# Kernel optimization log

Measured on AMD Instinct MI355X. Metric: run time of the kernel, lower is better.

## Reference

```python
import jax, jax.numpy as jnp
import numpy as np

N, F_IN, F_OUT, MAX_ORDER = 8192, 128, 128, 2
EDGE_DENSITY = 0.004  # avg degree ~33


def setup_inputs() -> dict:
    key = jax.random.key(0)
    k1, k2, k3, k4 = jax.random.split(key, 4)
    x = jax.random.normal(k1, (N, F_IN), dtype=jnp.float32)
    # dense stack of adjacency powers; layer only cares about the nonzero pattern
    adj_powers = (jax.random.uniform(k2, (MAX_ORDER, N, N)) < EDGE_DENSITY).astype(jnp.float32)
    edge_index = jax.random.randint(k3, (2, 32768), 0, N, dtype=jnp.int64)  # unused by the math
    W = jax.random.normal(k4, (F_IN, F_OUT), dtype=jnp.float32) / np.sqrt(F_IN).astype(np.float32)
    b = jnp.zeros((F_OUT,), dtype=jnp.float32)
    alpha = jnp.ones((MAX_ORDER,), dtype=jnp.float32)
    return {"x": x, "edge_index": edge_index, "adj_powers": adj_powers,
            "W": W, "b": b, "alpha": alpha}


def reference(x, edge_index, adj_powers, W, b, alpha):
    # GCNConv with shared (W, b) applied to each adjacency power's edge set.
    # dense->sparse->dense roundtrip in the original just binarizes the adjacency
    # (every nonzero entry becomes a unit-weight edge).
    xw = x @ W  # [N, F_out], shared across orders
    n = x.shape[0]
    diag = jnp.arange(n)

    def one_order(adj_n):
        A = (adj_n != 0).astype(x.dtype)
        # add_remaining_self_loops with unit weight == force diagonal to 1
        A = A.at[diag, diag].set(1.0)
        deg = A.sum(axis=1)  # [N]
        dinv = jnp.where(deg > 0, jax.lax.rsqrt(deg), 0.0)
        Ahat = dinv[:, None] * A * dinv[None, :]  # D^{-1/2} (A+I) D^{-1/2}
        return Ahat @ xw + b  # [N, F_out]

    per_order = jax.vmap(one_order)(adj_powers)  # [max_order, N, F_out]
    return jnp.einsum("o,onf->nf", alpha, per_order)
```

## Files before the change

kernel.cpp:

```cpp
#include <hip/hip_runtime.h>
#include <math.h>

#define NN 8192
#define FF 128
#define ORD 2
#define CSR_STRIDE 128
#define XW_ROWS 16
#define XW_BLOCKS (NN / XW_ROWS)
#define SCAN_BLOCKS (ORD * NN)

__global__ __launch_bounds__(256) void scan_xw_kernel(
    const float* __restrict__ adj, const float* __restrict__ x,
    const float* __restrict__ W,
    float* __restrict__ xw, float* __restrict__ dinv,
    int* __restrict__ cnt, int* __restrict__ colidx, int csr_ok)
{
    const int t = threadIdx.x;

    if (blockIdx.x < XW_BLOCKS) {
        const int row0 = blockIdx.x * XW_ROWS;
        __shared__ float xsT[FF * 20];
        for (int idx = t; idx < XW_ROWS * FF; idx += 256) {
            const int r = idx >> 7, k = idx & 127;
            xsT[k * 20 + r] = x[(size_t)(row0 + r) * FF + k];
        }
        __syncthreads();
        const int f = t & 127;
        const int h = t >> 7;
        float acc[8];
#pragma unroll
        for (int r = 0; r < 8; ++r) acc[r] = 0.f;
#pragma unroll 4
        for (int k = 0; k < FF; ++k) {
            const float wk = W[k * FF + f];
            const float4* xp = (const float4*)&xsT[k * 20 + h * 8];
            const float4 a0 = xp[0], a1 = xp[1];
            acc[0] += a0.x * wk; acc[1] += a0.y * wk;
            acc[2] += a0.z * wk; acc[3] += a0.w * wk;
            acc[4] += a1.x * wk; acc[5] += a1.y * wk;
            acc[6] += a1.z * wk; acc[7] += a1.w * wk;
        }
#pragma unroll
        for (int r = 0; r < 8; ++r)
            xw[(size_t)(row0 + h * 8 + r) * FF + f] = acc[r];
        return;
    }

    const int bid = blockIdx.x - XW_BLOCKS;
    const int i   = bid & (NN - 1);

    const float4* row = (const float4*)(adj + (size_t)bid * NN);

    unsigned int m = 0;
#pragma unroll
    for (int s = 0; s < 8; ++s) {
        const float4 v = row[s * 256 + t];
        if (v.x != 0.f) m |= 1u << (4 * s + 0);
        if (v.y != 0.f) m |= 1u << (4 * s + 1);
        if (v.z != 0.f) m |= 1u << (4 * s + 2);
        if (v.w != 0.f) m |= 1u << (4 * s + 3);
    }
    if (t == ((i >> 2) & 255)) m &= ~(1u << (((i >> 2) >> 8) * 4 + (i & 3)));

    const int c = __popc(m);

    const int lane = t & 63;
    int incl = c;
#pragma unroll
    for (int d = 1; d < 64; d <<= 1) {
        const int n = __shfl_up(incl, d);
        if (lane >= d) incl += n;
    }
    __shared__ int wtot[4];
    if (lane == 63) wtot[t >> 6] = incl;
    __syncthreads();
    const int w = t >> 6;
    int woff = 0;
#pragma unroll
    for (int ww = 0; ww < 3; ++ww)
        if (ww < w) woff += wtot[ww];
    const int total = wtot[0] + wtot[1] + wtot[2] + wtot[3];
    const int myoff = woff + incl - c;

    if (t == 0) {
        cnt[bid]  = total;
        dinv[bid] = 1.0f / sqrtf((float)(total + 1));
    }

    if (csr_ok && total <= CSR_STRIDE) {
        int* outp = colidx + (size_t)bid * CSR_STRIDE + myoff;
        unsigned int mm = m;
        const int base = 4 * t;
        while (mm) {
            const int b = __builtin_ctz(mm);
            mm &= mm - 1;
            *outp++ = ((b >> 2) << 10) + base + (b & 3);
        }
    }
}

__global__ __launch_bounds__(512) void gather_kernel(
    const float* __restrict__ adj, const float* __restrict__ xw,
    const float* __restrict__ dinv, const int* __restrict__ cnt,
    const int* __restrict__ colidx, const float* __restrict__ bias,
    const float* __restrict__ alpha, float* __restrict__ out, int csr_ok)
{
    const int i = blockIdx.x;
    const int t = threadIdx.x;
    const int l = t & 31;
    const int g = t >> 5;

    __shared__ int    qj[2 * CSR_STRIDE];
    __shared__ float  qw[2 * CSR_STRIDE];
    __shared__ float4 part[16][32];

    const int   c0 = cnt[i],        c1 = cnt[NN + i];
    const float di0 = dinv[i],      di1 = dinv[NN + i];
    const float a0 = alpha[0],      a1 = alpha[1];
    const int   ctot = c0 + c1;
    const int   fits = csr_ok && (c0 <= CSR_STRIDE) && (c1 <= CSR_STRIDE);

    float4 acc = make_float4(0.f, 0.f, 0.f, 0.f);

    if (fits) {
        if (t < ctot) {
            const int o = (t < c0) ? 0 : 1;
            const int e = (o == 0) ? t : t - c0;
            const int j = colidx[(size_t)(o * NN + i) * CSR_STRIDE + e];
            qj[t] = j;
            qw[t] = ((o == 0) ? a0 * di0 : a1 * di1) * dinv[o * NN + j];
        }
        __syncthreads();
        for (int e = g; e < ctot; e += 16) {
            const int   j = qj[e];
            const float w = qw[e];
            const float4 v = *(const float4*)&xw[(size_t)j * FF + 4 * l];
            acc.x += w * v.x; acc.y += w * v.y;
            acc.z += w * v.z; acc.w += w * v.w;
        }
    } else {
        for (int o = 0; o < ORD; ++o) {
            const float  wo   = (o == 0) ? a0 * di0 : a1 * di1;
            const float* rowp = adj + (size_t)(o * NN + i) * NN;
            for (int j = g * (NN / 16); j < (g + 1) * (NN / 16); ++j) {
                const float a = rowp[j];
                if (a != 0.f && j != i) {
                    const float w = wo * dinv[o * NN + j];
                    const float4 v = *(const float4*)&xw[(size_t)j * FF + 4 * l];
                    acc.x += w * v.x; acc.y += w * v.y;
                    acc.z += w * v.z; acc.w += w * v.w;
                }
            }
        }
    }

    part[g][l] = acc;
    __syncthreads();

    if (t < 32) {
        float4 r = part[0][t];
#pragma unroll
        for (int gg = 1; gg < 16; ++gg) {
            const float4 p = part[gg][t];
            r.x += p.x; r.y += p.y; r.z += p.z; r.w += p.w;
        }
        const float coefd = a0 * di0 * di0 + a1 * di1 * di1;
        const float cb    = a0 + a1;
        const float4 xi = *(const float4*)&xw[(size_t)i * FF + 4 * t];
        const float4 bb = *(const float4*)&bias[4 * t];
        r.x += coefd * xi.x + cb * bb.x;
        r.y += coefd * xi.y + cb * bb.y;
        r.z += coefd * xi.z + cb * bb.z;
        r.w += coefd * xi.w + cb * bb.w;
        *(float4*)&out[(size_t)i * FF + 4 * t] = r;
    }
}

extern "C" void kernel_launch(void* const* d_in, const int* in_sizes, int n_in,
                              void* d_out, int out_size, void* d_ws, size_t ws_size,
                              hipStream_t stream) {
    const float* x     = (const float*)d_in[0];
    const float* adj   = (const float*)d_in[2];
    const float* W     = (const float*)d_in[3];
    const float* bias  = (const float*)d_in[4];
    const float* alpha = (const float*)d_in[5];
    float* out         = (float*)d_out;

    char* ws = (char*)d_ws;
    size_t off = 0;
    float* xw     = (float*)(ws + off); off += (size_t)NN * FF * sizeof(float);
    float* dinv   = (float*)(ws + off); off += (size_t)ORD * NN * sizeof(float);
    int*   cnt    = (int*)(ws + off);   off += (size_t)ORD * NN * sizeof(int);
    int*   colidx = (int*)(ws + off);   off += (size_t)ORD * NN * CSR_STRIDE * sizeof(int);
    const int csr_ok = (ws_size >= off) ? 1 : 0;

    hipLaunchKernelGGL(scan_xw_kernel, dim3(XW_BLOCKS + SCAN_BLOCKS), dim3(256), 0, stream,
                       adj, x, W, xw, dinv, cnt, colidx, csr_ok);
    hipLaunchKernelGGL(gather_kernel, dim3(NN), dim3(512), 0, stream,
                       adj, xw, dinv, cnt, colidx, bias, alpha, out, csr_ok);
}
```

Measured before the change: 129.4 us.

## Scan adjacency per wave with persistent rows and gather bf16 xw copy

The adjacency scan moves from one 256-thread block per row to one 64-lane wave per row. It runs on 1024 persistent blocks that each loop over four rows and use only wave-level shuffles, so block barriers go away and each lane keeps more loads in flight. The xw kernel now also writes a bf16 copy of xw, and the gather kernel reads neighbour rows from that copy with 256 threads each handling 8 features. This halves gather traffic but adds rounding error. The final cross-group reduction becomes a tree through shared memory, which adds several barriers.

Result: faster. 125.5 us (-3.0%).

```diff
diff --git a/kernel.cpp b/kernel.cpp
--- a/kernel.cpp
+++ b/kernel.cpp
@@ -7,13 +7,23 @@
 #define CSR_STRIDE 128
 #define XW_ROWS 16
 #define XW_BLOCKS (NN / XW_ROWS)
-#define SCAN_BLOCKS (ORD * NN)
-
-__global__ __launch_bounds__(256) void scan_xw_kernel(
+#define SCAN_BLOCKS 1024
+#define ROWS_PER_WAVE 4
+#define NWAVES (SCAN_BLOCKS * 4)
+
+__device__ __forceinline__ unsigned short f2bf(float v) {
+    const unsigned int u = __float_as_uint(v);
+    return (unsigned short)((u + 0x7FFFu + ((u >> 16) & 1u)) >> 16);
+}
+__device__ __forceinline__ float bflo(unsigned int u) { return __uint_as_float(u << 16); }
+__device__ __forceinline__ float bfhi(unsigned int u) { return __uint_as_float(u & 0xFFFF0000u); }
+
+__global__ __launch_bounds__(256) void kernelA(
     const float* __restrict__ adj, const float* __restrict__ x,
     const float* __restrict__ W,
-    float* __restrict__ xw, float* __restrict__ dinv,
-    int* __restrict__ cnt, int* __restrict__ colidx, int csr_ok)
+    float* __restrict__ xw, unsigned short* __restrict__ xwh,
+    float* __restrict__ dinv, int* __restrict__ cnt,
+    int* __restrict__ colidx, int csr_ok)
 {
     const int t = threadIdx.x;
 
@@ -41,86 +51,106 @@
             acc[6] += a1.z * wk; acc[7] += a1.w * wk;
         }
 #pragma unroll
-        for (int r = 0; r < 8; ++r)
-            xw[(size_t)(row0 + h * 8 + r) * FF + f] = acc[r];
+        for (int r = 0; r < 8; ++r) {
+            const size_t idx = (size_t)(row0 + h * 8 + r) * FF + f;
+            xw[idx]  = acc[r];
+            xwh[idx] = f2bf(acc[r]);
+        }
         return;
     }
 
-    const int bid = blockIdx.x - XW_BLOCKS;
-    const int i   = bid & (NN - 1);
-
-    const float4* row = (const float4*)(adj + (size_t)bid * NN);
-
-    unsigned int m = 0;
-#pragma unroll
-    for (int s = 0; s < 8; ++s) {
-        const float4 v = row[s * 256 + t];
-        if (v.x != 0.f) m |= 1u << (4 * s + 0);
-        if (v.y != 0.f) m |= 1u << (4 * s + 1);
-        if (v.z != 0.f) m |= 1u << (4 * s + 2);
-        if (v.w != 0.f) m |= 1u << (4 * s + 3);
-    }
-    if (t == ((i >> 2) & 255)) m &= ~(1u << (((i >> 2) >> 8) * 4 + (i & 3)));
-
-    const int c = __popc(m);
-
+    const int wave_id = (blockIdx.x - XW_BLOCKS) * 4 + (t >> 6);
     const int lane = t & 63;
-    int incl = c;
-#pragma unroll
-    for (int d = 1; d < 64; d <<= 1) {
-        const int n = __shfl_up(incl, d);
-        if (lane >= d) incl += n;
-    }
-    __shared__ int wtot[4];
-    if (lane == 63) wtot[t >> 6] = incl;
-    __syncthreads();
-    const int w = t >> 6;
-    int woff = 0;
-#pragma unroll
-    for (int ww = 0; ww < 3; ++ww)
-        if (ww < w) woff += wtot[ww];
-    const int total = wtot[0] + wtot[1] + wtot[2] + wtot[3];
-    const int myoff = woff + incl - c;
-
-    if (t == 0) {
-        cnt[bid]  = total;
-        dinv[bid] = 1.0f / sqrtf((float)(total + 1));
-    }
-
-    if (csr_ok && total <= CSR_STRIDE) {
-        int* outp = colidx + (size_t)bid * CSR_STRIDE + myoff;
-        unsigned int mm = m;
-        const int base = 4 * t;
-        while (mm) {
-            const int b = __builtin_ctz(mm);
-            mm &= mm - 1;
-            *outp++ = ((b >> 2) << 10) + base + (b & 3);
-        }
-    }
-}
-
-__global__ __launch_bounds__(512) void gather_kernel(
+    const int b4l  = 4 * lane;
+
+#pragma unroll 1
+    for (int k = 0; k < ROWS_PER_WAVE; ++k) {
+        const int r = k * NWAVES + wave_id;
+        const int i = r & (NN - 1);
+        const float4* rowp = (const float4*)(adj + (size_t)r * NN);
+
+        unsigned int m[4];
+#pragma unroll
+        for (int ch = 0; ch < 4; ++ch) {
+            float4 v[8];
+#pragma unroll
+            for (int s = 0; s < 8; ++s) v[s] = rowp[ch * 512 + s * 64 + lane];
+            unsigned int mm = 0;
+#pragma unroll
+            for (int s = 0; s < 8; ++s) {
+                if (v[s].x != 0.f) mm |= 1u << (4 * s + 0);
+                if (v[s].y != 0.f) mm |= 1u << (4 * s + 1);
+                if (v[s].z != 0.f) mm |= 1u << (4 * s + 2);
+                if (v[s].w != 0.f) mm |= 1u << (4 * s + 3);
+            }
+            m[ch] = mm;
+        }
+
+        {
+            const int p_i    = i >> 2;
+            const int lane_i = p_i & 63;
+            const int ch_i   = p_i >> 9;
+            const unsigned int bit = 1u << (4 * ((p_i >> 6) & 7) + (i & 3));
+#pragma unroll
+            for (int ch = 0; ch < 4; ++ch)
+                if (ch == ch_i && lane == lane_i) m[ch] &= ~bit;
+        }
+
+        const int c = __popc(m[0]) + __popc(m[1]) + __popc(m[2]) + __popc(m[3]);
+
+        int incl = c;
+#pragma unroll
+        for (int d = 1; d < 64; d <<= 1) {
+            const int n = __shfl_up(incl, d);
+            if (lane >= d) incl += n;
+        }
+        const int total = __shfl(incl, 63);
+
+        if (lane == 0) {
+            cnt[r]  = total;
+            dinv[r] = 1.0f / sqrtf((float)(total + 1));
+        }
+
+        if (csr_ok && total <= CSR_STRIDE) {
+            int* outp = colidx + (size_t)r * CSR_STRIDE + (incl - c);
+#pragma unroll
+            for (int ch = 0; ch < 4; ++ch) {
+                unsigned int mm = m[ch];
+                while (mm) {
+                    const int bq = __builtin_ctz(mm);
+                    mm &= mm - 1;
+                    *outp++ = ch * 2048 + ((bq >> 2) << 8) + b4l + (bq & 3);
+                }
+            }
+        }
+    }
+}
+
+__global__ __launch_bounds__(256) void kernelB(
     const float* __restrict__ adj, const float* __restrict__ xw,
+    const unsigned short* __restrict__ xwh,
     const float* __restrict__ dinv, const int* __restrict__ cnt,
     const int* __restrict__ colidx, const float* __restrict__ bias,
     const float* __restrict__ alpha, float* __restrict__ out, int csr_ok)
 {
-    const int i = blockIdx.x;
-    const int t = threadIdx.x;
-    const int l = t & 31;
-    const int g = t >> 5;
-
-    __shared__ int    qj[2 * CSR_STRIDE];
-    __shared__ float  qw[2 * CSR_STRIDE];
-    __shared__ float4 part[16][32];
-
-    const int   c0 = cnt[i],        c1 = cnt[NN + i];
-    const float di0 = dinv[i],      di1 = dinv[NN + i];
-    const float a0 = alpha[0],      a1 = alpha[1];
+    const int i  = blockIdx.x;
+    const int t  = threadIdx.x;
+    const int fb = t & 15;
+    const int g  = t >> 4;
+
+    __shared__ int   qj[2 * CSR_STRIDE];
+    __shared__ float qw[2 * CSR_STRIDE];
+    __shared__ float part[16][16][8];
+
+    const int   c0  = cnt[i],  c1  = cnt[NN + i];
+    const float di0 = dinv[i], di1 = dinv[NN + i];
+    const float a0  = alpha[0], a1 = alpha[1];
     const int   ctot = c0 + c1;
     const int   fits = csr_ok && (c0 <= CSR_STRIDE) && (c1 <= CSR_STRIDE);
 
-    float4 acc = make_float4(0.f, 0.f, 0.f, 0.f);
+    float acc[8];
+#pragma unroll
+    for (int c = 0; c < 8; ++c) acc[c] = 0.f;
 
     if (fits) {
         if (t < ctot) {
@@ -134,9 +164,11 @@
         for (int e = g; e < ctot; e += 16) {
             const int   j = qj[e];
             const float w = qw[e];
-            const float4 v = *(const float4*)&xw[(size_t)j * FF + 4 * l];
-            acc.x += w * v.x; acc.y += w * v.y;
-            acc.z += w * v.z; acc.w += w * v.w;
+            const uint4 u = *(const uint4*)&xwh[(size_t)j * FF + 8 * fb];
+            acc[0] += w * bflo(u.x); acc[1] += w * bfhi(u.x);
+            acc[2] += w * bflo(u.y); acc[3] += w * bfhi(u.y);
+            acc[4] += w * bflo(u.z); acc[5] += w * bfhi(u.z);
+            acc[6] += w * bflo(u.w); acc[7] += w * bfhi(u.w);
         }
     } else {
         for (int o = 0; o < ORD; ++o) {
@@ -146,33 +178,38 @@
                 const float a = rowp[j];
                 if (a != 0.f && j != i) {
                     const float w = wo * dinv[o * NN + j];
-                    const float4 v = *(const float4*)&xw[(size_t)j * FF + 4 * l];
-                    acc.x += w * v.x; acc.y += w * v.y;
-                    acc.z += w * v.z; acc.w += w * v.w;
+                    const float* xr = &xw[(size_t)j * FF + 8 * fb];
+#pragma unroll
+                    for (int c = 0; c < 8; ++c) acc[c] += w * xr[c];
                 }
             }
         }
     }
 
-    part[g][l] = acc;
+#pragma unroll
+    for (int c = 0; c < 8; ++c) part[g][fb][c] = acc[c];
     __syncthreads();
 
-    if (t < 32) {
-        float4 r = part[0][t];
-#pragma unroll
-        for (int gg = 1; gg < 16; ++gg) {
-            const float4 p = part[gg][t];
-            r.x += p.x; r.y += p.y; r.z += p.z; r.w += p.w;
-        }
+#pragma unroll
+    for (int step = 8; step >= 1; step >>= 1) {
+        if (g < step) {
+#pragma unroll
+            for (int c = 0; c < 8; ++c) part[g][fb][c] += part[g + step][fb][c];
+        }
+        __syncthreads();
+    }
+
+    if (t < 16) {
         const float coefd = a0 * di0 * di0 + a1 * di1 * di1;
         const float cb    = a0 + a1;
-        const float4 xi = *(const float4*)&xw[(size_t)i * FF + 4 * t];
-        const float4 bb = *(const float4*)&bias[4 * t];
-        r.x += coefd * xi.x + cb * bb.x;
-        r.y += coefd * xi.y + cb * bb.y;
-        r.z += coefd * xi.z + cb * bb.z;
-        r.w += coefd * xi.w + cb * bb.w;
-        *(float4*)&out[(size_t)i * FF + 4 * t] = r;
+        const float* xi = &xw[(size_t)i * FF + 8 * t];
+        const float* bb = &bias[8 * t];
+        float r[8];
+#pragma unroll
+        for (int c = 0; c < 8; ++c)
+            r[c] = part[0][t][c] + coefd * xi[c] + cb * bb[c];
+        *(float4*)&out[(size_t)i * FF + 8 * t]     = make_float4(r[0], r[1], r[2], r[3]);
+        *(float4*)&out[(size_t)i * FF + 8 * t + 4] = make_float4(r[4], r[5], r[6], r[7]);
     }
 }
 
@@ -188,14 +225,15 @@
 
     char* ws = (char*)d_ws;
     size_t off = 0;
-    float* xw     = (float*)(ws + off); off += (size_t)NN * FF * sizeof(float);
-    float* dinv   = (float*)(ws + off); off += (size_t)ORD * NN * sizeof(float);
-    int*   cnt    = (int*)(ws + off);   off += (size_t)ORD * NN * sizeof(int);
-    int*   colidx = (int*)(ws + off);   off += (size_t)ORD * NN * CSR_STRIDE * sizeof(int);
+    float*          xw     = (float*)(ws + off); off += (size_t)NN * FF * sizeof(float);
+    unsigned short* xwh    = (unsigned short*)(ws + off); off += (size_t)NN * FF * sizeof(short);
+    float*          dinv   = (float*)(ws + off); off += (size_t)ORD * NN * sizeof(float);
+    int*            cnt    = (int*)(ws + off);   off += (size_t)ORD * NN * sizeof(int);
+    int*            colidx = (int*)(ws + off);   off += (size_t)ORD * NN * CSR_STRIDE * sizeof(int);
     const int csr_ok = (ws_size >= off) ? 1 : 0;
 
-    hipLaunchKernelGGL(scan_xw_kernel, dim3(XW_BLOCKS + SCAN_BLOCKS), dim3(256), 0, stream,
-                       adj, x, W, xw, dinv, cnt, colidx, csr_ok);
-    hipLaunchKernelGGL(gather_kernel, dim3(NN), dim3(512), 0, stream,
-                       adj, xw, dinv, cnt, colidx, bias, alpha, out, csr_ok);
-}
+    hipLaunchKernelGGL(kernelA, dim3(XW_BLOCKS + SCAN_BLOCKS), dim3(256), 0, stream,
+                       adj, x, W, xw, xwh, dinv, cnt, colidx, csr_ok);
+    hipLaunchKernelGGL(kernelB, dim3(NN), dim3(256), 0, stream,
+                       adj, xw, xwh, dinv, cnt, colidx, bias, alpha, out, csr_ok);
+}
```
